# Kernel optimization log

Measured on AMD Instinct MI355X. Metric: run time of the kernel, lower is better.

Reference implementation:

```python
import jax, jax.numpy as jnp
import numpy as np

N = 50000        # nodes
E = 800000       # original edges (no self loops)
HEADS = 2
OUT = 64         # hidden_channels
NUM_GRAPHS = 128
NEG_SLOPE = 0.2


def setup_inputs() -> dict:
    key = jax.random.key(0)
    ks = jax.random.split(key, 16)
    # edge_index guaranteed free of self loops (remove_self_loops then add_self_loops
    # in the original makes the final edge set = original edges + N self loops)
    src = jax.random.randint(ks[0], (E,), 0, N)
    off = jax.random.randint(ks[1], (E,), 1, N)
    dst = (src + off) % N
    edge_index = jnp.stack([src, dst]).astype(jnp.int64)
    batch = jnp.sort(jax.random.randint(ks[2], (N,), 0, NUM_GRAPHS)).astype(jnp.int64)
    def glorot(k, shape):
        fan = shape[-1] + (shape[0] if len(shape) > 1 else shape[-1])
        s = jnp.sqrt(6.0 / fan)
        return jax.random.uniform(k, shape, jnp.float32, -s, s)
    return {
        "x": jax.random.normal(ks[3], (N, 128), jnp.float32),
        "edge_index": edge_index,
        "batch": batch,
        "node_centrality": jax.random.uniform(ks[4], (N,), jnp.float32),
        "edge_centrality": jax.random.uniform(ks[5], (E,), jnp.float32),
        "W0": glorot(ks[6], (128, HEADS * OUT)),
        "as0": glorot(ks[7], (HEADS, OUT)),
        "ad0": glorot(ks[8], (HEADS, OUT)),
        "b0": jnp.ones((HEADS * OUT,), jnp.float32),
        "W1": glorot(ks[9], (HEADS * OUT, HEADS * OUT)),
        "as1": glorot(ks[10], (HEADS, OUT)),
        "ad1": glorot(ks[11], (HEADS, OUT)),
        "b1": jnp.ones((HEADS * OUT,), jnp.float32),
        "Wc": glorot(ks[12], (HEADS * OUT, 10)),
        "bc": jnp.zeros((10,), jnp.float32),
    }


def qgat_layer(x, src, dst, norm_quantum, W, a_src, a_dst, b):
    # x: [N, Cin]; src/dst: [E+N]; norm_quantum: [E+N]
    h = (x @ W).reshape(N, HEADS, OUT)                      # [N,H,D]
    alpha_s = jnp.einsum('nhd,hd->nh', h, a_src)            # [N,H]
    alpha_d = jnp.einsum('nhd,hd->nh', h, a_dst)
    alpha = jax.nn.leaky_relu(alpha_s[src] + alpha_d[dst], NEG_SLOPE)  # [E+N,H]
    # segment softmax over destination node (every node has a self loop)
    amax = jax.ops.segment_max(alpha, dst, num_segments=N)
    amax = jnp.where(jnp.isfinite(amax), amax, 0.0)
    ex = jnp.exp(alpha - amax[dst])
    denom = jax.ops.segment_sum(ex, dst, num_segments=N)
    attn = ex / (denom[dst] + 1e-16)                        # [E+N,H]
    # message: norm_quantum * alpha * x_j, scatter-add to dst
    msg = norm_quantum[:, None, None] * attn[:, :, None] * h[src]
    out = jax.ops.segment_sum(msg, dst, num_segments=N)     # [N,H,D]
    return jax.nn.relu(out.reshape(N, HEADS * OUT) + b)


def reference(x, edge_index, batch, node_centrality, edge_centrality,
              W0, as0, ad0, b0, W1, as1, ad1, b1, Wc, bc):
    loop = jnp.arange(N, dtype=edge_index.dtype)
    src = jnp.concatenate([edge_index[0], loop])            # self loops appended
    dst = jnp.concatenate([edge_index[1], loop])
    nq = jnp.concatenate([edge_centrality, node_centrality])  # [E+N]
    # eval mode: dropout is identity
    h = qgat_layer(x, src, dst, nq, W0, as0, ad0, b0)
    h = qgat_layer(h, src, dst, nq, W1, as1, ad1, b1)
    # global mean pool over graphs in the batch
    sums = jax.ops.segment_sum(h, batch, num_segments=NUM_GRAPHS)
    cnts = jax.ops.segment_sum(jnp.ones((N,), h.dtype), batch, num_segments=NUM_GRAPHS)
    pooled = sums / jnp.maximum(cnts, 1.0)[:, None]         # [G, H*D]
    return pooled @ Wc + bc                                  # [G, 10]
```

## Files before the change

### kernel.cpp

```cpp
#include <hip/hip_runtime.h>

#define N_NODES 50000
#define E_EDGES 800000
#define EA (E_EDGES + N_NODES)
#define NG 128
#define NEG 0.2f
#define NB_SCAN ((N_NODES + 255) / 256)

typedef _Float16 half8  __attribute__((ext_vector_type(8)));
typedef _Float16 half2t __attribute__((ext_vector_type(2)));
typedef float    floatx4 __attribute__((ext_vector_type(4)));

__device__ __forceinline__ half2t h2bits(unsigned u) { return __builtin_bit_cast(half2t, u); }

__global__ void init_kernel(const float* __restrict__ W0, const float* __restrict__ W1,
                            _Float16* __restrict__ Wt0, _Float16* __restrict__ Wt1,
                            int* __restrict__ deg) {
    int i = blockIdx.x * 256 + threadIdx.x;
    if (i < N_NODES) deg[i] = 0;
    if (i < 16384) {
        int c = i >> 7, k = i & 127;
        Wt0[c * 128 + k] = (_Float16)W0[k * 128 + c];
        Wt1[c * 128 + k] = (_Float16)W1[k * 128 + c];
    }
}

__global__ void hist_kernel(const int* __restrict__ ei, int* __restrict__ deg,
                            int* __restrict__ rank) {
    int e = blockIdx.x * blockDim.x + threadIdx.x;
    if (e >= EA) return;
    int d = (e < E_EDGES) ? ei[E_EDGES + e] : (e - E_EDGES);
    rank[e] = atomicAdd(&deg[d], 1);
}

__global__ void partial_kernel(const int* __restrict__ deg, int* __restrict__ part) {
    __shared__ int buf[4];
    int i = blockIdx.x * 256 + threadIdx.x;
    int v = (i < N_NODES) ? deg[i] : 0;
    for (int o = 32; o; o >>= 1) v += __shfl_xor(v, o);
    if ((threadIdx.x & 63) == 0) buf[threadIdx.x >> 6] = v;
    __syncthreads();
    if (threadIdx.x == 0) part[blockIdx.x] = buf[0] + buf[1] + buf[2] + buf[3];
}

__global__ void rowstart_kernel(const int* __restrict__ deg, const int* __restrict__ part,
                                int* __restrict__ rowstart) {
    __shared__ int buf[256];
    __shared__ int wsum[4];
    __shared__ int offs;
    int t = threadIdx.x;
    int pv = (t < blockIdx.x) ? part[t] : 0;
    for (int o = 32; o; o >>= 1) pv += __shfl_xor(pv, o);
    if ((t & 63) == 0) wsum[t >> 6] = pv;
    __syncthreads();
    if (t == 0) offs = wsum[0] + wsum[1] + wsum[2] + wsum[3];
    int i = blockIdx.x * 256 + t;
    int v = (i < N_NODES) ? deg[i] : 0;
    buf[t] = v;
    __syncthreads();
    for (int o = 1; o < 256; o <<= 1) {
        int u = (t >= o) ? buf[t - o] : 0;
        __syncthreads();
        buf[t] += u;
        __syncthreads();
    }
    if (i < N_NODES) rowstart[i] = offs + buf[t] - v;
    if (i == N_NODES - 1) rowstart[N_NODES] = offs + buf[t];
}

__global__ void build_kernel(const int* __restrict__ ei, const float* __restrict__ ec,
                             const float* __restrict__ nc, const int* __restrict__ rowstart,
                             const int* __restrict__ rank, uint2* __restrict__ csr2) {
    int e = blockIdx.x * blockDim.x + threadIdx.x;
    if (e >= EA) return;
    int s, d; float nq;
    if (e < E_EDGES) { s = ei[e]; d = ei[E_EDGES + e]; nq = ec[e]; }
    else             { s = e - E_EDGES; d = s; nq = nc[s]; }
    csr2[rowstart[d] + rank[e]] = make_uint2((unsigned)s, __float_as_uint(nq));
}

template<int SRC_F32>
__global__ __launch_bounds__(256) void gemm_mfma(const void* __restrict__ Xsrc,
                                                 const _Float16* __restrict__ Wt,
                                                 const float* __restrict__ as_,
                                                 const float* __restrict__ ad_,
                                                 unsigned* __restrict__ Hb,
                                                 float* __restrict__ als,
                                                 float* __restrict__ ald) {
    __shared__ _Float16 As[64][136];
    __shared__ _Float16 Bs[128 * 128];
    __shared__ float als_s[4][64];
    __shared__ float ald_s[4][64];
    const int tid = threadIdx.x;
    const int row0 = blockIdx.x * 64;

    if (SRC_F32) {
        const float* X = (const float*)Xsrc;
        for (int i = 0; i < 8; ++i) {
            int idx = tid + i * 256;
            int r = idx >> 5, q = idx & 31;
            int gr = row0 + r;
            float4 v = make_float4(0.f, 0.f, 0.f, 0.f);
            if (gr < N_NODES) v = ((const float4*)X)[(size_t)gr * 32 + q];
            half2t p0 = { (_Float16)v.x, (_Float16)v.y };
            half2t p1 = { (_Float16)v.z, (_Float16)v.w };
            *(half2t*)&As[r][q * 4]     = p0;
            *(half2t*)&As[r][q * 4 + 2] = p1;
        }
    } else {
        const uint4* X = (const uint4*)Xsrc;
        for (int i = 0; i < 4; ++i) {
            int idx = tid + i * 256;
            int r = idx >> 4, q = idx & 15;
            int gr = row0 + r;
            uint4 v = make_uint4(0u, 0u, 0u, 0u);
            if (gr < N_NODES) v = X[(size_t)gr * 16 + q];
            *(uint4*)&As[r][q * 8] = v;
        }
    }
    for (int i = 0; i < 8; ++i) {
        int idx = tid + i * 256;
        int r = idx >> 4, q = idx & 15;
        *(uint4*)&Bs[r * 128 + ((q ^ (r & 15)) << 3)] = ((const uint4*)Wt)[r * 16 + q];
    }
    __syncthreads();

    const int l = tid & 63, wv = tid >> 6;
    const int c0w = wv * 32;
    const int lr = l & 15, lq = l >> 4;

    floatx4 acc[4][2];
#pragma unroll
    for (int m = 0; m < 4; ++m)
#pragma unroll
        for (int n = 0; n < 2; ++n) acc[m][n] = (floatx4){0.f, 0.f, 0.f, 0.f};

#pragma unroll
    for (int kk = 0; kk < 4; ++kk) {
        int kb = kk * 32 + lq * 8;
        int kg = (kk * 4 + lq) ^ lr;
        half8 a0 = *(const half8*)&As[lr][kb];
        half8 a1 = *(const half8*)&As[16 + lr][kb];
        half8 a2 = *(const half8*)&As[32 + lr][kb];
        half8 a3 = *(const half8*)&As[48 + lr][kb];
        half8 b0 = *(const half8*)&Bs[(c0w + lr) * 128 + (kg << 3)];
        half8 b1 = *(const half8*)&Bs[(c0w + 16 + lr) * 128 + (kg << 3)];
        acc[0][0] = __builtin_amdgcn_mfma_f32_16x16x32_f16(a0, b0, acc[0][0], 0, 0, 0);
        acc[1][0] = __builtin_amdgcn_mfma_f32_16x16x32_f16(a1, b0, acc[1][0], 0, 0, 0);
        acc[2][0] = __builtin_amdgcn_mfma_f32_16x16x32_f16(a2, b0, acc[2][0], 0, 0, 0);
        acc[3][0] = __builtin_amdgcn_mfma_f32_16x16x32_f16(a3, b0, acc[3][0], 0, 0, 0);
        acc[0][1] = __builtin_amdgcn_mfma_f32_16x16x32_f16(a0, b1, acc[0][1], 0, 0, 0);
        acc[1][1] = __builtin_amdgcn_mfma_f32_16x16x32_f16(a1, b1, acc[1][1], 0, 0, 0);
        acc[2][1] = __builtin_amdgcn_mfma_f32_16x16x32_f16(a2, b1, acc[2][1], 0, 0, 0);
        acc[3][1] = __builtin_amdgcn_mfma_f32_16x16x32_f16(a3, b1, acc[3][1], 0, 0, 0);
    }

    __syncthreads();

    float asv0 = as_[c0w + lr],      adv0 = ad_[c0w + lr];
    float asv1 = as_[c0w + 16 + lr], adv1 = ad_[c0w + 16 + lr];
#pragma unroll
    for (int m = 0; m < 4; ++m) {
#pragma unroll
        for (int reg = 0; reg < 4; ++reg) {
            float v0 = acc[m][0][reg];
            float v1 = acc[m][1][reg];
            int rl = 16 * m + 4 * lq + reg;
            _Float16* rowp = &As[rl][0];
            rowp[c0w + lr]      = (_Float16)v0;
            rowp[c0w + 16 + lr] = (_Float16)v1;
            float ss = v0 * asv0 + v1 * asv1;
            float dd = v0 * adv0 + v1 * adv1;
            ss += __shfl_xor(ss, 1); dd += __shfl_xor(dd, 1);
            ss += __shfl_xor(ss, 2); dd += __shfl_xor(dd, 2);
            ss += __shfl_xor(ss, 4); dd += __shfl_xor(dd, 4);
            ss += __shfl_xor(ss, 8); dd += __shfl_xor(dd, 8);
            if (lr == 0) { als_s[wv][rl] = ss; ald_s[wv][rl] = dd; }
        }
    }
    __syncthreads();

    for (int i = 0; i < 4; ++i) {
        int idx = tid + i * 256;
        int r = idx >> 4, q = idx & 15;
        int grow = row0 + r;
        if (grow < N_NODES) {
            uint4 v = *(uint4*)((unsigned short*)&As[r][0] + q * 8);
            ((uint4*)Hb)[(size_t)grow * 16 + q] = v;
        }
    }
    int r = tid & 63, sel = tid >> 6;
    int grow = row0 + r;
    if (grow < N_NODES) {
        if (sel == 0)      als[grow * 2 + 0] = als_s[0][r] + als_s[1][r];
        else if (sel == 1) als[grow * 2 + 1] = als_s[2][r] + als_s[3][r];
        else if (sel == 2) ald[grow * 2 + 0] = ald_s[0][r] + ald_s[1][r];
        else               ald[grow * 2 + 1] = ald_s[2][r] + ald_s[3][r];
    }
}

__global__ __launch_bounds__(256) void agg_kernel(const uint4* __restrict__ Hb4,
                                                  const uint2* __restrict__ csr2,
                                                  const float* __restrict__ als,
                                                  const float* __restrict__ ald,
                                                  const int* __restrict__ rowstart,
                                                  const float* __restrict__ bias,
                                                  _Float16* __restrict__ outp) {
    __shared__ uint4 sw[4][64];
    const int wv = threadIdx.x >> 6;
    int n = blockIdx.x * 4 + wv;
    if (n >= N_NODES) return;
    const int lane = threadIdx.x & 63;
    int start = rowstart[n], end = rowstart[n + 1];
    int deg = end - start;
    const float2* als2 = (const float2*)als;
    float2 adn = ((const float2*)ald)[n];

    int   s_reg  = n;
    float nq_reg = 0.f, a0_reg = -1e30f, a1_reg = -1e30f;
    if (lane < deg) {
        uint2 v = csr2[start + lane];
        s_reg  = (int)v.x;
        nq_reg = __uint_as_float(v.y);
        float2 av = als2[s_reg];
        float a0 = av.x + adn.x; a0_reg = (a0 > 0.f) ? a0 : NEG * a0;
        float a1 = av.y + adn.y; a1_reg = (a1 > 0.f) ? a1 : NEG * a1;
    }
    float m0 = a0_reg, m1 = a1_reg;
    for (int i = start + 64 + lane; i < end; i += 64) {
        uint2 v = csr2[i];
        float2 av = als2[v.x];
        float a0 = av.x + adn.x; a0 = (a0 > 0.f) ? a0 : NEG * a0;
        float a1 = av.y + adn.y; a1 = (a1 > 0.f) ? a1 : NEG * a1;
        m0 = fmaxf(m0, a0); m1 = fmaxf(m1, a1);
    }
    for (int o = 32; o; o >>= 1) { m0 = fmaxf(m0, __shfl_xor(m0, o)); m1 = fmaxf(m1, __shfl_xor(m1, o)); }

    float e0 = __expf(a0_reg - m0), e1 = __expf(a1_reg - m1);
    float s0 = e0, s1 = e1;
    for (int i = start + 64 + lane; i < end; i += 64) {
        uint2 v = csr2[i];
        float2 av = als2[v.x];
        float a0 = av.x + adn.x; a0 = (a0 > 0.f) ? a0 : NEG * a0;
        float a1 = av.y + adn.y; a1 = (a1 > 0.f) ? a1 : NEG * a1;
        s0 += __expf(a0 - m0); s1 += __expf(a1 - m1);
    }
    for (int o = 32; o; o >>= 1) { s0 += __shfl_xor(s0, o); s1 += __shfl_xor(s1, o); }
    float inv0 = 1.f / (s0 + 1e-16f), inv1 = 1.f / (s1 + 1e-16f);

    sw[wv][lane] = make_uint4((unsigned)s_reg,
                              __float_as_uint(nq_reg * e0 * inv0),
                              __float_as_uint(nq_reg * e1 * inv1), 0u);

    const int  c16   = lane & 15;
    const int  g     = lane >> 4;
    const bool head0 = (c16 < 8);
    float acc0 = 0.f, acc1 = 0.f, acc2 = 0.f, acc3 = 0.f;
    float acc4 = 0.f, acc5 = 0.f, acc6 = 0.f, acc7 = 0.f;
    int cnt4 = (deg < 64) ? ((deg + 3) & ~3) : 64;
#pragma unroll 4
    for (int jp = 0; jp < cnt4; jp += 4) {
        uint4 sv = sw[wv][jp + g];
        float w  = __uint_as_float(head0 ? sv.y : sv.z);
        uint4 hv = Hb4[(size_t)(sv.x * 16u + (unsigned)c16)];
        half2t h0 = h2bits(hv.x), h1 = h2bits(hv.y), h2 = h2bits(hv.z), h3 = h2bits(hv.w);
        acc0 += (float)h0.x * w; acc1 += (float)h0.y * w;
        acc2 += (float)h1.x * w; acc3 += (float)h1.y * w;
        acc4 += (float)h2.x * w; acc5 += (float)h2.y * w;
        acc6 += (float)h3.x * w; acc7 += (float)h3.y * w;
    }
    for (int cbase = start + 64; cbase < end; cbase += 64) {
        int   s2 = n; float w0f = 0.f, w1f = 0.f;
        int i = cbase + lane;
        if (i < end) {
            uint2 v = csr2[i];
            s2 = (int)v.x;
            float nq = __uint_as_float(v.y);
            float2 av = als2[s2];
            float a0 = av.x + adn.x; a0 = (a0 > 0.f) ? a0 : NEG * a0;
            float a1 = av.y + adn.y; a1 = (a1 > 0.f) ? a1 : NEG * a1;
            w0f = nq * __expf(a0 - m0) * inv0;
            w1f = nq * __expf(a1 - m1) * inv1;
        }
        sw[wv][lane] = make_uint4((unsigned)s2, __float_as_uint(w0f), __float_as_uint(w1f), 0u);
        int rem = end - cbase; if (rem > 64) rem = 64;
        int r4 = (rem + 3) & ~3;
        for (int jp = 0; jp < r4; jp += 4) {
            uint4 sv = sw[wv][jp + g];
            float w  = __uint_as_float(head0 ? sv.y : sv.z);
            uint4 hv = Hb4[(size_t)(sv.x * 16u + (unsigned)c16)];
            half2t h0 = h2bits(hv.x), h1 = h2bits(hv.y), h2 = h2bits(hv.z), h3 = h2bits(hv.w);
            acc0 += (float)h0.x * w; acc1 += (float)h0.y * w;
            acc2 += (float)h1.x * w; acc3 += (float)h1.y * w;
            acc4 += (float)h2.x * w; acc5 += (float)h2.y * w;
            acc6 += (float)h3.x * w; acc7 += (float)h3.y * w;
        }
    }
    acc0 += __shfl_xor(acc0, 16); acc1 += __shfl_xor(acc1, 16);
    acc2 += __shfl_xor(acc2, 16); acc3 += __shfl_xor(acc3, 16);
    acc4 += __shfl_xor(acc4, 16); acc5 += __shfl_xor(acc5, 16);
    acc6 += __shfl_xor(acc6, 16); acc7 += __shfl_xor(acc7, 16);
    acc0 += __shfl_xor(acc0, 32); acc1 += __shfl_xor(acc1, 32);
    acc2 += __shfl_xor(acc2, 32); acc3 += __shfl_xor(acc3, 32);
    acc4 += __shfl_xor(acc4, 32); acc5 += __shfl_xor(acc5, 32);
    acc6 += __shfl_xor(acc6, 32); acc7 += __shfl_xor(acc7, 32);

    if (g == 0) {
        float4 ba = ((const float4*)bias)[c16 * 2];
        float4 bb = ((const float4*)bias)[c16 * 2 + 1];
        float o0 = acc0 + ba.x; o0 = o0 > 0.f ? o0 : 0.f;
        float o1 = acc1 + ba.y; o1 = o1 > 0.f ? o1 : 0.f;
        float o2 = acc2 + ba.z; o2 = o2 > 0.f ? o2 : 0.f;
        float o3 = acc3 + ba.w; o3 = o3 > 0.f ? o3 : 0.f;
        float o4 = acc4 + bb.x; o4 = o4 > 0.f ? o4 : 0.f;
        float o5 = acc5 + bb.y; o5 = o5 > 0.f ? o5 : 0.f;
        float o6 = acc6 + bb.z; o6 = o6 > 0.f ? o6 : 0.f;
        float o7 = acc7 + bb.w; o7 = o7 > 0.f ? o7 : 0.f;
        half8 hv = { (_Float16)o0, (_Float16)o1, (_Float16)o2, (_Float16)o3,
                     (_Float16)o4, (_Float16)o5, (_Float16)o6, (_Float16)o7 };
        *(half8*)(outp + (size_t)n * 128 + 8 * c16) = hv;
    }
}

__global__ __launch_bounds__(256) void poolcls_kernel(const half2t* __restrict__ Obh,
                                                      const int* __restrict__ batch,
                                                      const float* __restrict__ Wc,
                                                      const float* __restrict__ bc,
                                                      float* __restrict__ outp) {
    int g = blockIdx.x;
    int lo = 0, hi = N_NODES;
    while (lo < hi) { int mid = (lo + hi) >> 1; if (batch[mid] < g) lo = mid + 1; else hi = mid; }
    int start = lo;
    hi = N_NODES;
    while (lo < hi) { int mid = (lo + hi) >> 1; if (batch[mid] <= g) lo = mid + 1; else hi = mid; }
    int end = lo;

    int c2 = threadIdx.x & 63;
    int r4 = threadIdx.x >> 6;
    float a0 = 0.f, a1 = 0.f;
    for (int i = start + r4; i < end; i += 4) {
        half2t hv = Obh[(size_t)i * 64 + c2];
        a0 += (float)hv.x;
        a1 += (float)hv.y;
    }
    __shared__ float2 red[4][64];
    __shared__ float p[128];
    red[r4][c2].x = a0; red[r4][c2].y = a1;
    __syncthreads();
    if (threadIdx.x < 64) {
        int t = threadIdx.x;
        float inv = 1.f / fmaxf((float)(end - start), 1.f);
        float2 r0 = red[0][t], r1 = red[1][t], r2 = red[2][t], r3 = red[3][t];
        p[2 * t]     = (r0.x + r1.x + r2.x + r3.x) * inv;
        p[2 * t + 1] = (r0.y + r1.y + r2.y + r3.y) * inv;
    }
    __syncthreads();
    if (threadIdx.x < 10) {
        float acc = bc[threadIdx.x];
        for (int k = 0; k < 128; ++k) acc += p[k] * Wc[k * 10 + threadIdx.x];
        outp[g * 10 + threadIdx.x] = acc;
    }
}

extern "C" void kernel_launch(void* const* d_in, const int* in_sizes, int n_in,
                              void* d_out, int out_size, void* d_ws, size_t ws_size,
                              hipStream_t stream) {
    const float* x     = (const float*)d_in[0];
    const int*   ei    = (const int*)d_in[1];
    const int*   batch = (const int*)d_in[2];
    const float* nc    = (const float*)d_in[3];
    const float* ec    = (const float*)d_in[4];
    const float* W0    = (const float*)d_in[5];
    const float* as0   = (const float*)d_in[6];
    const float* ad0   = (const float*)d_in[7];
    const float* b0    = (const float*)d_in[8];
    const float* W1    = (const float*)d_in[9];
    const float* as1   = (const float*)d_in[10];
    const float* ad1   = (const float*)d_in[11];
    const float* b1    = (const float*)d_in[12];
    const float* Wc    = (const float*)d_in[13];
    const float* bc    = (const float*)d_in[14];
    float* out = (float*)d_out;

    char* ws = (char*)d_ws;
    size_t off = 0;
    auto alloc = [&](size_t bytes) { void* p = ws + off; off += (bytes + 255) & ~size_t(255); return p; };
    unsigned*  Hb       = (unsigned*)alloc(sizeof(unsigned) * N_NODES * 64);
    _Float16*  Xh       = (_Float16*)alloc(sizeof(_Float16) * N_NODES * 128);
    _Float16*  Ob       = (_Float16*)alloc(sizeof(_Float16) * N_NODES * 128);
    float*     als      = (float*)alloc(sizeof(float) * N_NODES * 2);
    float*     ald      = (float*)alloc(sizeof(float) * N_NODES * 2);
    _Float16*  Wt0      = (_Float16*)alloc(sizeof(_Float16) * 128 * 128);
    _Float16*  Wt1      = (_Float16*)alloc(sizeof(_Float16) * 128 * 128);
    int*       deg      = (int*)alloc(sizeof(int) * N_NODES);
    int*       rank     = (int*)alloc(sizeof(int) * EA);
    int*       part     = (int*)alloc(sizeof(int) * NB_SCAN);
    int*       rowstart = (int*)alloc(sizeof(int) * (N_NODES + 1));
    uint2*     csr2     = (uint2*)alloc(sizeof(uint2) * EA);

    init_kernel<<<NB_SCAN, 256, 0, stream>>>(W0, W1, Wt0, Wt1, deg);
    hist_kernel<<<(EA + 255) / 256, 256, 0, stream>>>(ei, deg, rank);
    partial_kernel<<<NB_SCAN, 256, 0, stream>>>(deg, part);
    rowstart_kernel<<<NB_SCAN, 256, 0, stream>>>(deg, part, rowstart);
    build_kernel<<<(EA + 255) / 256, 256, 0, stream>>>(ei, ec, nc, rowstart, rank, csr2);

    int gemm_grid   = (N_NODES + 63) / 64;
    int nwaveblocks = (N_NODES + 3) / 4;

    gemm_mfma<1><<<gemm_grid, 256, 0, stream>>>(x, Wt0, as0, ad0, Hb, als, ald);
    agg_kernel<<<nwaveblocks, 256, 0, stream>>>((const uint4*)Hb, csr2, als, ald, rowstart, b0, Xh);

    gemm_mfma<0><<<gemm_grid, 256, 0, stream>>>(Xh, Wt1, as1, ad1, Hb, als, ald);
    agg_kernel<<<nwaveblocks, 256, 0, stream>>>((const uint4*)Hb, csr2, als, ald, rowstart, b1, Ob);

    poolcls_kernel<<<NG, 256, 0, stream>>>((const half2t*)Ob, batch, Wc, bc, out);
}
```

Before: 213.0 us.

## Split pooling into chunked atomic partial sums and a separate classifier kernel

Global mean pooling used to run as 128 blocks, one per graph, each walking about 390 rows serially. It now runs as many 64-row chunk blocks that accumulate per-graph partial sums and flush them with float atomics. A second small kernel then computes counts by binary search, normalises, and applies the classifier. This exposes more parallelism in the pooling stage, at the cost of an extra launch, atomic traffic, and non-deterministic summation order.

```diff
diff --git a/kernel.cpp b/kernel.cpp
--- a/kernel.cpp
+++ b/kernel.cpp
@@ -6,6 +6,7 @@
 #define NG 128
 #define NEG 0.2f
 #define NB_SCAN ((N_NODES + 255) / 256)
+#define PCH 64
 
 typedef _Float16 half8  __attribute__((ext_vector_type(8)));
 typedef _Float16 half2t __attribute__((ext_vector_type(2)));
@@ -15,9 +16,10 @@
 
 __global__ void init_kernel(const float* __restrict__ W0, const float* __restrict__ W1,
                             _Float16* __restrict__ Wt0, _Float16* __restrict__ Wt1,
-                            int* __restrict__ deg) {
+                            int* __restrict__ deg, float* __restrict__ sums) {
     int i = blockIdx.x * 256 + threadIdx.x;
     if (i < N_NODES) deg[i] = 0;
+    if (i < NG * 128) sums[i] = 0.f;
     if (i < 16384) {
         int c = i >> 7, k = i & 127;
         Wt0[c * 128 + k] = (_Float16)W0[k * 128 + c];
@@ -322,38 +324,51 @@
     }
 }
 
-__global__ __launch_bounds__(256) void poolcls_kernel(const half2t* __restrict__ Obh,
-                                                      const int* __restrict__ batch,
-                                                      const float* __restrict__ Wc,
-                                                      const float* __restrict__ bc,
-                                                      float* __restrict__ outp) {
-    int g = blockIdx.x;
-    int lo = 0, hi = N_NODES;
-    while (lo < hi) { int mid = (lo + hi) >> 1; if (batch[mid] < g) lo = mid + 1; else hi = mid; }
-    int start = lo;
-    hi = N_NODES;
-    while (lo < hi) { int mid = (lo + hi) >> 1; if (batch[mid] <= g) lo = mid + 1; else hi = mid; }
-    int end = lo;
-
+__global__ __launch_bounds__(256) void pool_partial(const half2t* __restrict__ Obh,
+                                                    const int* __restrict__ batch,
+                                                    float* __restrict__ sums) {
+    int row0 = blockIdx.x * PCH;
     int c2 = threadIdx.x & 63;
     int r4 = threadIdx.x >> 6;
+    int end = row0 + PCH; if (end > N_NODES) end = N_NODES;
     float a0 = 0.f, a1 = 0.f;
-    for (int i = start + r4; i < end; i += 4) {
+    int curg = -1;
+    for (int i = row0 + r4; i < end; i += 4) {
+        int g = batch[i];
+        if (g != curg) {
+            if (curg >= 0) {
+                atomicAdd(&sums[curg * 128 + 2 * c2],     a0);
+                atomicAdd(&sums[curg * 128 + 2 * c2 + 1], a1);
+            }
+            a0 = 0.f; a1 = 0.f; curg = g;
+        }
         half2t hv = Obh[(size_t)i * 64 + c2];
         a0 += (float)hv.x;
         a1 += (float)hv.y;
     }
-    __shared__ float2 red[4][64];
+    if (curg >= 0) {
+        atomicAdd(&sums[curg * 128 + 2 * c2],     a0);
+        atomicAdd(&sums[curg * 128 + 2 * c2 + 1], a1);
+    }
+}
+
+__global__ void cls_kernel(const float* __restrict__ sums, const int* __restrict__ batch,
+                           const float* __restrict__ Wc, const float* __restrict__ bc,
+                           float* __restrict__ outp) {
+    int g = blockIdx.x;
     __shared__ float p[128];
-    red[r4][c2].x = a0; red[r4][c2].y = a1;
-    __syncthreads();
-    if (threadIdx.x < 64) {
-        int t = threadIdx.x;
-        float inv = 1.f / fmaxf((float)(end - start), 1.f);
-        float2 r0 = red[0][t], r1 = red[1][t], r2 = red[2][t], r3 = red[3][t];
-        p[2 * t]     = (r0.x + r1.x + r2.x + r3.x) * inv;
-        p[2 * t + 1] = (r0.y + r1.y + r2.y + r3.y) * inv;
-    }
+    __shared__ int cnt_s;
+    if (threadIdx.x == 0) {
+        int lo = 0, hi = N_NODES;
+        while (lo < hi) { int mid = (lo + hi) >> 1; if (batch[mid] < g) lo = mid + 1; else hi = mid; }
+        int start = lo;
+        hi = N_NODES;
+        while (lo < hi) { int mid = (lo + hi) >> 1; if (batch[mid] <= g) lo = mid + 1; else hi = mid; }
+        cnt_s = lo - start;
+    }
+    __syncthreads();
+    float inv = 1.f / fmaxf((float)cnt_s, 1.f);
+    p[threadIdx.x] = sums[g * 128 + threadIdx.x] * inv;
     __syncthreads();
     if (threadIdx.x < 10) {
         float acc = bc[threadIdx.x];
@@ -397,8 +412,9 @@
     int*       part     = (int*)alloc(sizeof(int) * NB_SCAN);
     int*       rowstart = (int*)alloc(sizeof(int) * (N_NODES + 1));
     uint2*     csr2     = (uint2*)alloc(sizeof(uint2) * EA);
-
-    init_kernel<<<NB_SCAN, 256, 0, stream>>>(W0, W1, Wt0, Wt1, deg);
+    float*     sums     = (float*)alloc(sizeof(float) * NG * 128);
+
+    init_kernel<<<NB_SCAN, 256, 0, stream>>>(W0, W1, Wt0, Wt1, deg, sums);
     hist_kernel<<<(EA + 255) / 256, 256, 0, stream>>>(ei, deg, rank);
     partial_kernel<<<NB_SCAN, 256, 0, stream>>>(deg, part);
     rowstart_kernel<<<NB_SCAN, 256, 0, stream>>>(deg, part, rowstart);
@@ -413,5 +429,6 @@
     gemm_mfma<0><<<gemm_grid, 256, 0, stream>>>(Xh, Wt1, as1, ad1, Hb, als, ald);
     agg_kernel<<<nwaveblocks, 256, 0, stream>>>((const uint4*)Hb, csr2, als, ald, rowstart, b1, Ob);
 
-    poolcls_kernel<<<NG, 256, 0, stream>>>((const half2t*)Ob, batch, Wc, bc, out);
-}
+    pool_partial<<<(N_NODES + PCH - 1) / PCH, 256, 0, stream>>>((const half2t*)Ob, batch, sums);
+    cls_kernel<<<NG, 128, 0, stream>>>(sums, batch, Wc, bc, out);
+}
```

Result: faster. 197.9 us, median of 2 (-7.1%).
